# Kernel tuning notes

Measured on AMD Instinct MI355X. Metric: run time of the kernel, lower is better.

Reference implementation:

```python
import jax, jax.numpy as jnp
import numpy as np

B, D = 65536, 512
E_SPEC, E_SH = 2, 2
H1, H2, EO, TH = 64, 32, 32, 64
T1_DIM, T2_DIM = 3, 2


def _lin(key, shape, fan_in):
    bound = 1.0 / np.sqrt(fan_in)
    return jax.random.uniform(key, shape, jnp.float32, -bound, bound)


def _expert_params(key, n):
    ks = jax.random.split(key, 6)
    return (
        _lin(ks[0], (n, D, H1), D), _lin(ks[1], (n, H1), D),
        _lin(ks[2], (n, H1, H2), H1), _lin(ks[3], (n, H2), H1),
        _lin(ks[4], (n, H2, EO), H2), _lin(ks[5], (n, EO), H2),
    )


def setup_inputs() -> dict:
    key = jax.random.key(0)
    ks = jax.random.split(key, 8)
    x = jax.random.normal(ks[0], (B, D), jnp.float32)
    sh = _expert_params(ks[1], E_SH)
    t1 = _expert_params(ks[2], E_SPEC)
    t2 = _expert_params(ks[3], E_SPEC)
    EG = E_SPEC + E_SH
    g1_W, g1_b = _lin(jax.random.fold_in(ks[4], 0), (D, EG), D), _lin(jax.random.fold_in(ks[4], 1), (EG,), D)
    g2_W, g2_b = _lin(jax.random.fold_in(ks[5], 0), (D, EG), D), _lin(jax.random.fold_in(ks[5], 1), (EG,), D)
    kt = jax.random.split(ks[6], 4)
    tw1_W1, tw1_b1 = _lin(kt[0], (EO, TH), EO), _lin(kt[1], (TH,), EO)
    tw1_W2, tw1_b2 = _lin(kt[2], (TH, T1_DIM), TH), _lin(kt[3], (T1_DIM,), TH)
    kt2 = jax.random.split(ks[7], 4)
    tw2_W1, tw2_b1 = _lin(kt2[0], (EO, TH), EO), _lin(kt2[1], (TH,), EO)
    tw2_W2, tw2_b2 = _lin(kt2[2], (TH, T2_DIM), TH), _lin(kt2[3], (T2_DIM,), TH)
    return {
        "x": x,
        "sh_W1": sh[0], "sh_b1": sh[1], "sh_W2": sh[2], "sh_b2": sh[3], "sh_W3": sh[4], "sh_b3": sh[5],
        "t1_W1": t1[0], "t1_b1": t1[1], "t1_W2": t1[2], "t1_b2": t1[3], "t1_W3": t1[4], "t1_b3": t1[5],
        "t2_W1": t2[0], "t2_b1": t2[1], "t2_W2": t2[2], "t2_b2": t2[3], "t2_W3": t2[4], "t2_b3": t2[5],
        "g1_W": g1_W, "g1_b": g1_b, "g2_W": g2_W, "g2_b": g2_b,
        "tw1_W1": tw1_W1, "tw1_b1": tw1_b1, "tw1_W2": tw1_W2, "tw1_b2": tw1_b2,
        "tw2_W1": tw2_W1, "tw2_b1": tw2_b1, "tw2_W2": tw2_W2, "tw2_b2": tw2_b2,
    }


def _experts(x, W1, b1, W2, b2, W3, b3):
    # batched over expert dim e: [e, B, h] (dropout is identity in eval)
    h = jax.nn.relu(jnp.einsum('bi,eih->ebh', x, W1) + b1[:, None, :])
    h = jax.nn.relu(jnp.einsum('ebh,ehk->ebk', h, W2) + b2[:, None, :])
    return jnp.einsum('ebk,eko->ebo', h, W3) + b3[:, None, :]


def _tower(g, W1, b1, W2, b2):
    return jax.nn.relu(g @ W1 + b1) @ W2 + b2


def reference(x, sh_W1, sh_b1, sh_W2, sh_b2, sh_W3, sh_b3,
              t1_W1, t1_b1, t1_W2, t1_b2, t1_W3, t1_b3,
              t2_W1, t2_b1, t2_W2, t2_b2, t2_W3, t2_b3,
              g1_W, g1_b, g2_W, g2_b,
              tw1_W1, tw1_b1, tw1_W2, tw1_b2,
              tw2_W1, tw2_b1, tw2_W2, tw2_b2):
    shared = _experts(x, sh_W1, sh_b1, sh_W2, sh_b2, sh_W3, sh_b3)   # [E_SH, B, EO]
    task1 = _experts(x, t1_W1, t1_b1, t1_W2, t1_b2, t1_W3, t1_b3)    # [E_SPEC, B, EO]
    task2 = _experts(x, t2_W1, t2_b1, t2_W2, t2_b2, t2_W3, t2_b3)

    sel1 = jax.nn.softmax(x @ g1_W + g1_b, axis=1)                    # [B, E_SPEC+E_SH]
    g1 = jnp.einsum('ebc,be->bc', jnp.concatenate([task1, shared], 0), sel1)
    o1 = _tower(g1, tw1_W1, tw1_b1, tw1_W2, tw1_b2)
    o1 = o1.at[:, 0].set(jax.nn.sigmoid(o1[:, 0]))
    o1 = o1.at[:, 2].set(jax.nn.sigmoid(o1[:, 2]))

    sel2 = jax.nn.softmax(x @ g2_W + g2_b, axis=1)
    g2 = jnp.einsum('ebc,be->bc', jnp.concatenate([task2, shared], 0), sel2)
    o2 = _tower(g2, tw2_W1, tw2_b1, tw2_W2, tw2_b2)
    o2 = o2.at[:, 1].set(jax.nn.sigmoid(o2[:, 1]))
    return (o1, o2)
```

## Files before the change

kernel.cpp:

```cpp
#include <hip/hip_runtime.h>
#include <hip/hip_bf16.h>


#define MT 32
#define NT1 25

typedef __bf16 bf16x8 __attribute__((ext_vector_type(8)));
typedef float f32x4 __attribute__((ext_vector_type(4)));

__device__ __forceinline__ unsigned short f2bf(float f) {
    unsigned u = __builtin_bit_cast(unsigned, f);
    return (unsigned short)((u + 0x7FFFu + ((u >> 16) & 1u)) >> 16);
}
__device__ __forceinline__ unsigned pk(float a, float b) {
    return (unsigned)f2bf(a) | ((unsigned)f2bf(b) << 16);
}

__global__ void pack_all(const float* __restrict__ sh_W1, const float* __restrict__ t1_W1,
                         const float* __restrict__ t2_W1, const float* __restrict__ g1_W,
                         const float* __restrict__ g2_W,
                         const float* __restrict__ sh_W2, const float* __restrict__ t1_W2,
                         const float* __restrict__ t2_W2,
                         const float* __restrict__ sh_W3, const float* __restrict__ t1_W3,
                         const float* __restrict__ t2_W3,
                         const float* __restrict__ sh_b1, const float* __restrict__ t1_b1,
                         const float* __restrict__ t2_b1,
                         const float* __restrict__ sh_b2, const float* __restrict__ t1_b2,
                         const float* __restrict__ t2_b2,
                         const float* __restrict__ sh_b3, const float* __restrict__ t1_b3,
                         const float* __restrict__ t2_b3,
                         const float* __restrict__ g1_b, const float* __restrict__ g2_b,
                         unsigned short* __restrict__ wf1, unsigned short* __restrict__ wf2,
                         unsigned short* __restrict__ wf3,
                         float* __restrict__ b1c, float* __restrict__ b2c, float* __restrict__ b3c) {
    int p0 = blockIdx.x * blockDim.x + threadIdx.x;
    if (p0 < 204800) {
        int p = p0;
        int j = p & 7, lane = (p >> 3) & 63, ks = (p >> 9) & 15, nt = p >> 13;
        int col = nt * 16 + (lane & 15);
        int k = ks * 32 + (lane >> 4) * 8 + j;
        float v = 0.f;
        if (col < 384) {
            int e = col >> 6, ci = col & 63;
            const float* W = (e < 2) ? t1_W1 : (e < 4) ? t2_W1 : sh_W1;
            v = W[((size_t)(e & 1) * 512 + k) * 64 + ci];
        } else if (col < 388) {
            v = g1_W[k * 4 + (col - 384)];
        } else if (col < 392) {
            v = g2_W[k * 4 + (col - 388)];
        }
        wf1[p] = f2bf(v);
        return;
    }
    int p = p0 - 204800;
    if (p < 12288) {
        int j = p & 7, lane = (p >> 3) & 63, ks = (p >> 9) & 1, nt = (p >> 10) & 1, e = p >> 11;
        int col = nt * 16 + (lane & 15);
        int k = ks * 32 + (lane >> 4) * 8 + j;
        const float* W = (e < 2) ? t1_W2 : (e < 4) ? t2_W2 : sh_W2;
        wf2[p] = f2bf(W[((size_t)(e & 1) * 64 + k) * 32 + col]);
    } else if (p < 18432) {
        int q = p - 12288;
        int j = q & 7, lane = (q >> 3) & 63, nt = (q >> 9) & 1, e = q >> 10;
        int col = nt * 16 + (lane & 15);
        int k = (lane >> 4) * 8 + j;
        const float* W = (e < 2) ? t1_W3 : (e < 4) ? t2_W3 : sh_W3;
        wf3[q] = f2bf(W[((size_t)(e & 1) * 32 + k) * 32 + col]);
    } else if (p < 18432 + 392) {
        int t = p - 18432;
        float v;
        if (t < 384) {
            int e = t >> 6, ci = t & 63;
            const float* bb = (e < 2) ? t1_b1 : (e < 4) ? t2_b1 : sh_b1;
            v = bb[(e & 1) * 64 + ci];
        } else if (t < 388) v = g1_b[t - 384];
        else v = g2_b[t - 388];
        b1c[t] = v;
    } else if (p < 18824 + 192) {
        int t = p - 18824;
        int e = t >> 5, ci = t & 31;
        const float* bb = (e < 2) ? t1_b2 : (e < 4) ? t2_b2 : sh_b2;
        b2c[t] = bb[(e & 1) * 32 + ci];
    } else if (p < 19016 + 192) {
        int t = p - 19016;
        int e = t >> 5, ci = t & 31;
        const float* bb = (e < 2) ? t1_b3 : (e < 4) ? t2_b3 : sh_b3;
        b3c[t] = bb[(e & 1) * 32 + ci];
    }
}

#define LDS_BYTES 48128

__global__ __launch_bounds__(512, 6) void ple_fused(
    const float* __restrict__ x,
    const unsigned short* __restrict__ wf1, const unsigned short* __restrict__ wf2,
    const unsigned short* __restrict__ wf3,
    const float* __restrict__ b1c, const float* __restrict__ b2c, const float* __restrict__ b3c,
    const float* __restrict__ tw1_W1, const float* __restrict__ tw1_b1,
    const float* __restrict__ tw1_W2, const float* __restrict__ tw1_b2,
    const float* __restrict__ tw2_W1, const float* __restrict__ tw2_b1,
    const float* __restrict__ tw2_W2, const float* __restrict__ tw2_b2,
    float* __restrict__ out, int ntok) {
    extern __shared__ char smem[];
    unsigned short* xlds = (unsigned short*)smem;
    unsigned short* h1 = (unsigned short*)smem;
    float* eo = (float*)smem;
    float* th1 = (float*)smem;
    float* th2 = (float*)(smem + 8448);
    unsigned short* h2 = (unsigned short*)(smem + 33280);
    float* g1l = (float*)(smem + 33280);
    float* g2l = (float*)(smem + 37504);
    float* gate = (float*)(smem + 46080);
    float* sel = (float*)(smem + 47104);

    const int tid = threadIdx.x;
    const int w = tid >> 6, l = tid & 63, r = l & 15, g = l >> 4;
    const int tok0 = blockIdx.x * MT;

    const float* xb = x + (size_t)tok0 * 512;
    float4 va[8];
#pragma unroll
    for (int i = 0; i < 4; ++i) {
        va[2 * i] = *(const float4*)(xb + i * 4096 + tid * 8);
        va[2 * i + 1] = *(const float4*)(xb + i * 4096 + tid * 8 + 4);
    }
#pragma unroll
    for (int i = 0; i < 4; ++i) {
        int f = i * 4096 + tid * 8;
        int tok = f >> 9, k = f & 511;
        float4 a = va[2 * i], b = va[2 * i + 1];
        *(uint4*)(&xlds[tok * 520 + k]) =
            make_uint4(pk(a.x, a.y), pk(a.z, a.w), pk(b.x, b.y), pk(b.z, b.w));
    }
    __syncthreads();

    int ntl[4] = {w, w + 8, w + 16, 24};
    const int ntn = (w == 7) ? 4 : 3;

    f32x4 acc[4][2];
#pragma unroll
    for (int i = 0; i < 4; ++i)
#pragma unroll
        for (int m = 0; m < 2; ++m) acc[i][m] = (f32x4){0.f, 0.f, 0.f, 0.f};

    const bf16x8* wf1v = (const bf16x8*)wf1;
#pragma unroll 4
    for (int ks = 0; ks < 16; ++ks) {
        bf16x8 bfr[4];
#pragma unroll
        for (int i = 0; i < 4; ++i)
            if (i < ntn) bfr[i] = wf1v[((ntl[i] * 16 + ks) << 6) + l];
        bf16x8 afr[2];
#pragma unroll
        for (int m = 0; m < 2; ++m)
            afr[m] = *(const bf16x8*)&xlds[(m * 16 + r) * 520 + ks * 32 + g * 8];
#pragma unroll
        for (int i = 0; i < 4; ++i)
            if (i < ntn)
#pragma unroll
                for (int m = 0; m < 2; ++m)
                    acc[i][m] = __builtin_amdgcn_mfma_f32_16x16x32_bf16(afr[m], bfr[i], acc[i][m], 0, 0, 0);
    }
    __syncthreads();

#pragma unroll
    for (int i = 0; i < 4; ++i)
        if (i < ntn) {
            int nt = ntl[i];
            if (nt < 24) {
#pragma unroll
                for (int m = 0; m < 2; ++m)
#pragma unroll
                    for (int q = 0; q < 4; ++q) {
                        int tokr = m * 16 + g * 4 + q;
                        int col = nt * 16 + r;
                        float v = acc[i][m][q] + b1c[col];
                        h1[tokr * 408 + col] = f2bf(fmaxf(v, 0.f));
                    }
            } else if (r < 8) {
#pragma unroll
                for (int m = 0; m < 2; ++m)
#pragma unroll
                    for (int q = 0; q < 4; ++q) {
                        int tokr = m * 16 + g * 4 + q;
                        gate[tokr * 8 + r] = acc[i][m][q] + b1c[384 + r];
                    }
            }
        }
    __syncthreads();

    if (tid < 32) {
#pragma unroll
        for (int gi = 0; gi < 2; ++gi) {
            float l0 = gate[tid * 8 + gi * 4 + 0];
            float l1 = gate[tid * 8 + gi * 4 + 1];
            float l2 = gate[tid * 8 + gi * 4 + 2];
            float l3 = gate[tid * 8 + gi * 4 + 3];
            float mx = fmaxf(fmaxf(l0, l1), fmaxf(l2, l3));
            float e0 = __expf(l0 - mx), e1 = __expf(l1 - mx);
            float e2 = __expf(l2 - mx), e3 = __expf(l3 - mx);
            float inv = 1.f / (e0 + e1 + e2 + e3);
            sel[tid * 8 + gi * 4 + 0] = e0 * inv;
            sel[tid * 8 + gi * 4 + 1] = e1 * inv;
            sel[tid * 8 + gi * 4 + 2] = e2 * inv;
            sel[tid * 8 + gi * 4 + 3] = e3 * inv;
        }
    }

    const int nj = (w < 4) ? 2 : 1;
    const int je[2] = {w >> 1, (w + 8) >> 1};
    const int jn[2] = {w & 1, w & 1};

    f32x4 acc2[2][2];
#pragma unroll
    for (int jj = 0; jj < 2; ++jj)
#pragma unroll
        for (int m = 0; m < 2; ++m) acc2[jj][m] = (f32x4){0.f, 0.f, 0.f, 0.f};

    const bf16x8* wf2v = (const bf16x8*)wf2;
#pragma unroll
    for (int jj = 0; jj < 2; ++jj)
        if (jj < nj) {
            int e = je[jj], nt2 = jn[jj];
#pragma unroll
            for (int ks = 0; ks < 2; ++ks) {
                bf16x8 bb = wf2v[(((e * 2 + nt2) * 2 + ks) << 6) + l];
#pragma unroll
                for (int m = 0; m < 2; ++m) {
                    bf16x8 aa = *(const bf16x8*)&h1[(m * 16 + r) * 408 + e * 64 + ks * 32 + g * 8];
                    acc2[jj][m] = __builtin_amdgcn_mfma_f32_16x16x32_bf16(aa, bb, acc2[jj][m], 0, 0, 0);
                }
            }
        }
#pragma unroll
    for (int jj = 0; jj < 2; ++jj)
        if (jj < nj) {
            int e = je[jj], nt2 = jn[jj];
#pragma unroll
            for (int m = 0; m < 2; ++m)
#pragma unroll
                for (int q = 0; q < 4; ++q) {
                    int tokr = m * 16 + g * 4 + q;
                    int col = nt2 * 16 + r;
                    float v = acc2[jj][m][q] + b2c[e * 32 + col];
                    h2[tokr * 200 + e * 32 + col] = f2bf(fmaxf(v, 0.f));
                }
        }
    __syncthreads();

    f32x4 acc3[2][2];
#pragma unroll
    for (int jj = 0; jj < 2; ++jj)
#pragma unroll
        for (int m = 0; m < 2; ++m) acc3[jj][m] = (f32x4){0.f, 0.f, 0.f, 0.f};

    const bf16x8* wf3v = (const bf16x8*)wf3;
#pragma unroll
    for (int jj = 0; jj < 2; ++jj)
        if (jj < nj) {
            int e = je[jj], nt2 = jn[jj];
            bf16x8 bb = wf3v[((e * 2 + nt2) << 6) + l];
#pragma unroll
            for (int m = 0; m < 2; ++m) {
                bf16x8 aa = *(const bf16x8*)&h2[(m * 16 + r) * 200 + e * 32 + g * 8];
                acc3[jj][m] = __builtin_amdgcn_mfma_f32_16x16x32_bf16(aa, bb, acc3[jj][m], 0, 0, 0);
            }
        }
#pragma unroll
    for (int jj = 0; jj < 2; ++jj)
        if (jj < nj) {
            int e = je[jj], nt2 = jn[jj];
#pragma unroll
            for (int m = 0; m < 2; ++m)
#pragma unroll
                for (int q = 0; q < 4; ++q) {
                    int tokr = m * 16 + g * 4 + q;
                    eo[(e * 32 + tokr) * 33 + nt2 * 16 + r] =
                        acc3[jj][m][q] + b3c[e * 32 + nt2 * 16 + r];
                }
        }
    __syncthreads();

    {
        int tok = tid >> 4, c0 = (tid & 15) * 2;
        float s[8];
#pragma unroll
        for (int i = 0; i < 8; ++i) s[i] = sel[tok * 8 + i];
#pragma unroll
        for (int c = 0; c < 2; ++c) {
            int cc = c0 + c;
            float e0 = eo[(0 * 32 + tok) * 33 + cc];
            float e1 = eo[(1 * 32 + tok) * 33 + cc];
            float e2 = eo[(2 * 32 + tok) * 33 + cc];
            float e3 = eo[(3 * 32 + tok) * 33 + cc];
            float e4 = eo[(4 * 32 + tok) * 33 + cc];
            float e5 = eo[(5 * 32 + tok) * 33 + cc];
            g1l[tok * 33 + cc] = s[0] * e0 + s[1] * e1 + s[2] * e4 + s[3] * e5;
            g2l[tok * 33 + cc] = s[4] * e2 + s[5] * e3 + s[6] * e4 + s[7] * e5;
        }
    }
    __syncthreads();

    {
        int tt = tid & 255, tower = tid >> 8;
        int tok = tt >> 3, h0 = (tt & 7) * 8;
        const float* W1 = tower ? tw2_W1 : tw1_W1;
        const float* B1 = tower ? tw2_b1 : tw1_b1;
        const float* gl = tower ? g2l : g1l;
        float* th = tower ? th2 : th1;
        float a[8];
#pragma unroll
        for (int hh = 0; hh < 8; ++hh) a[hh] = B1[h0 + hh];
        for (int c = 0; c < 32; ++c) {
            float gv = gl[tok * 33 + c];
#pragma unroll
            for (int hh = 0; hh < 8; ++hh)
                a[hh] += gv * W1[c * 64 + h0 + hh];
        }
#pragma unroll
        for (int hh = 0; hh < 8; ++hh)
            th[tok * 66 + h0 + hh] = fmaxf(a[hh], 0.f);
    }
    __syncthreads();

    if (tid < 128) {
        int tok = tid >> 2, jx = tid & 3;
        if (jx < 3) {
            float s = tw1_b2[jx];
            for (int hh = 0; hh < 64; ++hh) s += th1[tok * 66 + hh] * tw1_W2[hh * 3 + jx];
            if (jx != 1) s = 1.f / (1.f + __expf(-s));
            out[(size_t)(tok0 + tok) * 3 + jx] = s;
        }
    } else if (tid >= 256 && tid < 384) {
        int t2 = tid - 256, tok = t2 >> 2, jx = t2 & 3;
        if (jx < 2) {
            float s = tw2_b2[jx];
            for (int hh = 0; hh < 64; ++hh) s += th2[tok * 66 + hh] * tw2_W2[hh * 2 + jx];
            if (jx == 1) s = 1.f / (1.f + __expf(-s));
            out[(size_t)ntok * 3 + (size_t)(tok0 + tok) * 2 + jx] = s;
        }
    }
}

extern "C" void kernel_launch(void* const* d_in, const int* in_sizes, int n_in,
                              void* d_out, int out_size, void* d_ws, size_t ws_size,
                              hipStream_t stream) {
    const float* x = (const float*)d_in[0];
    const float* sh_W1 = (const float*)d_in[1];
    const float* sh_b1 = (const float*)d_in[2];
    const float* sh_W2 = (const float*)d_in[3];
    const float* sh_b2 = (const float*)d_in[4];
    const float* sh_W3 = (const float*)d_in[5];
    const float* sh_b3 = (const float*)d_in[6];
    const float* t1_W1 = (const float*)d_in[7];
    const float* t1_b1 = (const float*)d_in[8];
    const float* t1_W2 = (const float*)d_in[9];
    const float* t1_b2 = (const float*)d_in[10];
    const float* t1_W3 = (const float*)d_in[11];
    const float* t1_b3 = (const float*)d_in[12];
    const float* t2_W1 = (const float*)d_in[13];
    const float* t2_b1 = (const float*)d_in[14];
    const float* t2_W2 = (const float*)d_in[15];
    const float* t2_b2 = (const float*)d_in[16];
    const float* t2_W3 = (const float*)d_in[17];
    const float* t2_b3 = (const float*)d_in[18];
    const float* g1_W = (const float*)d_in[19];
    const float* g1_b = (const float*)d_in[20];
    const float* g2_W = (const float*)d_in[21];
    const float* g2_b = (const float*)d_in[22];
    const float* tw1_W1 = (const float*)d_in[23];
    const float* tw1_b1 = (const float*)d_in[24];
    const float* tw1_W2 = (const float*)d_in[25];
    const float* tw1_b2 = (const float*)d_in[26];
    const float* tw2_W1 = (const float*)d_in[27];
    const float* tw2_b1 = (const float*)d_in[28];
    const float* tw2_W2 = (const float*)d_in[29];
    const float* tw2_b2 = (const float*)d_in[30];

    unsigned short* wf1 = (unsigned short*)d_ws;
    unsigned short* wf2 = (unsigned short*)((char*)d_ws + 409600);
    unsigned short* wf3 = (unsigned short*)((char*)d_ws + 434176);
    float* b1c = (float*)((char*)d_ws + 446464);
    float* b2c = (float*)((char*)d_ws + 448032);
    float* b3c = (float*)((char*)d_ws + 448800);

    pack_all<<<438, 512, 0, stream>>>(sh_W1, t1_W1, t2_W1, g1_W, g2_W,
                                      sh_W2, t1_W2, t2_W2, sh_W3, t1_W3, t2_W3,
                                      sh_b1, t1_b1, t2_b1, sh_b2, t1_b2, t2_b2,
                                      sh_b3, t1_b3, t2_b3, g1_b, g2_b,
                                      wf1, wf2, wf3, b1c, b2c, b3c);

    (void)hipFuncSetAttribute((const void*)ple_fused,
                              hipFuncAttributeMaxDynamicSharedMemorySize, LDS_BYTES);

    int ntok = in_sizes[0] / 512;
    int nblk = ntok / MT;
    ple_fused<<<nblk, 512, LDS_BYTES, stream>>>(
        x, wf1, wf2, wf3, b1c, b2c, b3c,
        tw1_W1, tw1_b1, tw1_W2, tw1_b2, tw2_W1, tw2_b1, tw2_W2, tw2_b2,
        (float*)d_out, ntok);
}
```

Before: 310.4 us.

## Give each wave one expert's full MLP chain in private LDS slabs

Work is reassigned so each of six waves computes a whole expert (layer1→layer2→layer3) in its own LDS slab, and the two remaining waves compute the gate logits. This removes several block-wide barriers between the expert layers. The softmax is now computed redundantly per thread inside the mixing step instead of in a separate 32-thread phase. In exchange, LDS use grows enough that launch bounds drop from 6 to 4 blocks, and the waves carry uneven load: the gate waves do far less work than the expert waves.

```diff
diff --git a/kernel.cpp b/kernel.cpp
--- a/kernel.cpp
+++ b/kernel.cpp
@@ -89,9 +89,11 @@
     }
 }
 
-#define LDS_BYTES 48128
-
-__global__ __launch_bounds__(512, 6) void ple_fused(
+#define SLAB_OFF 33280
+#define SLAB_SZ  7168
+#define LDS_BYTES 77312
+
+__global__ __launch_bounds__(512, 4) void ple_fused(
     const float* __restrict__ x,
     const unsigned short* __restrict__ wf1, const unsigned short* __restrict__ wf2,
     const unsigned short* __restrict__ wf3,
@@ -103,200 +105,179 @@
     float* __restrict__ out, int ntok) {
     extern __shared__ char smem[];
     unsigned short* xlds = (unsigned short*)smem;
-    unsigned short* h1 = (unsigned short*)smem;
-    float* eo = (float*)smem;
-    float* th1 = (float*)smem;
-    float* th2 = (float*)(smem + 8448);
-    unsigned short* h2 = (unsigned short*)(smem + 33280);
-    float* g1l = (float*)(smem + 33280);
-    float* g2l = (float*)(smem + 37504);
-    float* gate = (float*)(smem + 46080);
-    float* sel = (float*)(smem + 47104);
+    float* gate = (float*)(smem + 76288);
+    float* g1l = (float*)smem;
+    float* g2l = (float*)(smem + 4224);
+    float* th1 = (float*)(smem + 8448);
+    float* th2 = (float*)(smem + 16896);
 
     const int tid = threadIdx.x;
     const int w = tid >> 6, l = tid & 63, r = l & 15, g = l >> 4;
     const int tok0 = blockIdx.x * MT;
 
-    const float* xb = x + (size_t)tok0 * 512;
-    float4 va[8];
-#pragma unroll
-    for (int i = 0; i < 4; ++i) {
-        va[2 * i] = *(const float4*)(xb + i * 4096 + tid * 8);
-        va[2 * i + 1] = *(const float4*)(xb + i * 4096 + tid * 8 + 4);
-    }
-#pragma unroll
-    for (int i = 0; i < 4; ++i) {
-        int f = i * 4096 + tid * 8;
-        int tok = f >> 9, k = f & 511;
-        float4 a = va[2 * i], b = va[2 * i + 1];
-        *(uint4*)(&xlds[tok * 520 + k]) =
-            make_uint4(pk(a.x, a.y), pk(a.z, a.w), pk(b.x, b.y), pk(b.z, b.w));
+    {
+        const float* xb = x + (size_t)tok0 * 512;
+        float4 va[8];
+#pragma unroll
+        for (int i = 0; i < 4; ++i) {
+            va[2 * i] = *(const float4*)(xb + i * 4096 + tid * 8);
+            va[2 * i + 1] = *(const float4*)(xb + i * 4096 + tid * 8 + 4);
+        }
+#pragma unroll
+        for (int i = 0; i < 4; ++i) {
+            int f = i * 4096 + tid * 8;
+            int tok = f >> 9, k = f & 511;
+            float4 a = va[2 * i], b = va[2 * i + 1];
+            *(uint4*)(&xlds[tok * 520 + k]) =
+                make_uint4(pk(a.x, a.y), pk(a.z, a.w), pk(b.x, b.y), pk(b.z, b.w));
+        }
     }
     __syncthreads();
 
-    int ntl[4] = {w, w + 8, w + 16, 24};
-    const int ntn = (w == 7) ? 4 : 3;
-
-    f32x4 acc[4][2];
-#pragma unroll
-    for (int i = 0; i < 4; ++i)
-#pragma unroll
-        for (int m = 0; m < 2; ++m) acc[i][m] = (f32x4){0.f, 0.f, 0.f, 0.f};
-
     const bf16x8* wf1v = (const bf16x8*)wf1;
+    if (w < 6) {
+        const int e = w;
+        unsigned short* h1w = (unsigned short*)(smem + SLAB_OFF + w * SLAB_SZ);
+        unsigned short* h2w = (unsigned short*)(smem + SLAB_OFF + w * SLAB_SZ + 4608);
+        float* eow = (float*)(smem + SLAB_OFF + w * SLAB_SZ);
+
+        f32x4 acc[4][2];
+#pragma unroll
+        for (int i = 0; i < 4; ++i)
+#pragma unroll
+            for (int m = 0; m < 2; ++m) acc[i][m] = (f32x4){0.f, 0.f, 0.f, 0.f};
+
 #pragma unroll 4
-    for (int ks = 0; ks < 16; ++ks) {
-        bf16x8 bfr[4];
-#pragma unroll
-        for (int i = 0; i < 4; ++i)
-            if (i < ntn) bfr[i] = wf1v[((ntl[i] * 16 + ks) << 6) + l];
-        bf16x8 afr[2];
-#pragma unroll
-        for (int m = 0; m < 2; ++m)
-            afr[m] = *(const bf16x8*)&xlds[(m * 16 + r) * 520 + ks * 32 + g * 8];
-#pragma unroll
-        for (int i = 0; i < 4; ++i)
-            if (i < ntn)
+        for (int ks = 0; ks < 16; ++ks) {
+            bf16x8 bfr[4];
+#pragma unroll
+            for (int i = 0; i < 4; ++i)
+                bfr[i] = wf1v[(((e * 4 + i) * 16 + ks) << 6) + l];
+            bf16x8 afr[2];
+#pragma unroll
+            for (int m = 0; m < 2; ++m)
+                afr[m] = *(const bf16x8*)&xlds[(m * 16 + r) * 520 + ks * 32 + g * 8];
+#pragma unroll
+            for (int i = 0; i < 4; ++i)
 #pragma unroll
                 for (int m = 0; m < 2; ++m)
                     acc[i][m] = __builtin_amdgcn_mfma_f32_16x16x32_bf16(afr[m], bfr[i], acc[i][m], 0, 0, 0);
-    }
-    __syncthreads();
-
-#pragma unroll
-    for (int i = 0; i < 4; ++i)
-        if (i < ntn) {
-            int nt = ntl[i];
-            if (nt < 24) {
+        }
+#pragma unroll
+        for (int i = 0; i < 4; ++i)
+#pragma unroll
+            for (int m = 0; m < 2; ++m)
+#pragma unroll
+                for (int q = 0; q < 4; ++q) {
+                    float v = acc[i][m][q] + b1c[e * 64 + i * 16 + r];
+                    h1w[(m * 16 + g * 4 + q) * 72 + i * 16 + r] = f2bf(fmaxf(v, 0.f));
+                }
+
+        const bf16x8* wf2v = (const bf16x8*)wf2;
+        f32x4 acc2[2][2];
+#pragma unroll
+        for (int i = 0; i < 2; ++i)
+#pragma unroll
+            for (int m = 0; m < 2; ++m) acc2[i][m] = (f32x4){0.f, 0.f, 0.f, 0.f};
+#pragma unroll
+        for (int ks = 0; ks < 2; ++ks) {
+            bf16x8 aa[2];
+#pragma unroll
+            for (int m = 0; m < 2; ++m)
+                aa[m] = *(const bf16x8*)&h1w[(m * 16 + r) * 72 + ks * 32 + g * 8];
+#pragma unroll
+            for (int i = 0; i < 2; ++i) {
+                bf16x8 bb = wf2v[(((e * 2 + i) * 2 + ks) << 6) + l];
 #pragma unroll
                 for (int m = 0; m < 2; ++m)
-#pragma unroll
-                    for (int q = 0; q < 4; ++q) {
-                        int tokr = m * 16 + g * 4 + q;
-                        int col = nt * 16 + r;
-                        float v = acc[i][m][q] + b1c[col];
-                        h1[tokr * 408 + col] = f2bf(fmaxf(v, 0.f));
-                    }
-            } else if (r < 8) {
+                    acc2[i][m] = __builtin_amdgcn_mfma_f32_16x16x32_bf16(aa[m], bb, acc2[i][m], 0, 0, 0);
+            }
+        }
+#pragma unroll
+        for (int i = 0; i < 2; ++i)
+#pragma unroll
+            for (int m = 0; m < 2; ++m)
+#pragma unroll
+                for (int q = 0; q < 4; ++q) {
+                    float v = acc2[i][m][q] + b2c[e * 32 + i * 16 + r];
+                    h2w[(m * 16 + g * 4 + q) * 40 + i * 16 + r] = f2bf(fmaxf(v, 0.f));
+                }
+
+        const bf16x8* wf3v = (const bf16x8*)wf3;
+        f32x4 acc3[2][2];
+#pragma unroll
+        for (int i = 0; i < 2; ++i)
+#pragma unroll
+            for (int m = 0; m < 2; ++m) acc3[i][m] = (f32x4){0.f, 0.f, 0.f, 0.f};
+        {
+            bf16x8 aa[2];
+#pragma unroll
+            for (int m = 0; m < 2; ++m)
+                aa[m] = *(const bf16x8*)&h2w[(m * 16 + r) * 40 + g * 8];
+#pragma unroll
+            for (int i = 0; i < 2; ++i) {
+                bf16x8 bb = wf3v[((e * 2 + i) << 6) + l];
 #pragma unroll
                 for (int m = 0; m < 2; ++m)
-#pragma unroll
-                    for (int q = 0; q < 4; ++q) {
-                        int tokr = m * 16 + g * 4 + q;
-                        gate[tokr * 8 + r] = acc[i][m][q] + b1c[384 + r];
-                    }
+                    acc3[i][m] = __builtin_amdgcn_mfma_f32_16x16x32_bf16(aa[m], bb, acc3[i][m], 0, 0, 0);
             }
         }
-    __syncthreads();
-
-    if (tid < 32) {
-#pragma unroll
-        for (int gi = 0; gi < 2; ++gi) {
-            float l0 = gate[tid * 8 + gi * 4 + 0];
-            float l1 = gate[tid * 8 + gi * 4 + 1];
-            float l2 = gate[tid * 8 + gi * 4 + 2];
-            float l3 = gate[tid * 8 + gi * 4 + 3];
-            float mx = fmaxf(fmaxf(l0, l1), fmaxf(l2, l3));
-            float e0 = __expf(l0 - mx), e1 = __expf(l1 - mx);
-            float e2 = __expf(l2 - mx), e3 = __expf(l3 - mx);
-            float inv = 1.f / (e0 + e1 + e2 + e3);
-            sel[tid * 8 + gi * 4 + 0] = e0 * inv;
-            sel[tid * 8 + gi * 4 + 1] = e1 * inv;
-            sel[tid * 8 + gi * 4 + 2] = e2 * inv;
-            sel[tid * 8 + gi * 4 + 3] = e3 * inv;
-        }
-    }
-
-    const int nj = (w < 4) ? 2 : 1;
-    const int je[2] = {w >> 1, (w + 8) >> 1};
-    const int jn[2] = {w & 1, w & 1};
-
-    f32x4 acc2[2][2];
-#pragma unroll
-    for (int jj = 0; jj < 2; ++jj)
-#pragma unroll
-        for (int m = 0; m < 2; ++m) acc2[jj][m] = (f32x4){0.f, 0.f, 0.f, 0.f};
-
-    const bf16x8* wf2v = (const bf16x8*)wf2;
-#pragma unroll
-    for (int jj = 0; jj < 2; ++jj)
-        if (jj < nj) {
-            int e = je[jj], nt2 = jn[jj];
-#pragma unroll
-            for (int ks = 0; ks < 2; ++ks) {
-                bf16x8 bb = wf2v[(((e * 2 + nt2) * 2 + ks) << 6) + l];
-#pragma unroll
-                for (int m = 0; m < 2; ++m) {
-                    bf16x8 aa = *(const bf16x8*)&h1[(m * 16 + r) * 408 + e * 64 + ks * 32 + g * 8];
-                    acc2[jj][m] = __builtin_amdgcn_mfma_f32_16x16x32_bf16(aa, bb, acc2[jj][m], 0, 0, 0);
-                }
-            }
-        }
-#pragma unroll
-    for (int jj = 0; jj < 2; ++jj)
-        if (jj < nj) {
-            int e = je[jj], nt2 = jn[jj];
-#pragma unroll
-            for (int m = 0; m < 2; ++m)
-#pragma unroll
-                for (int q = 0; q < 4; ++q) {
-                    int tokr = m * 16 + g * 4 + q;
-                    int col = nt2 * 16 + r;
-                    float v = acc2[jj][m][q] + b2c[e * 32 + col];
-                    h2[tokr * 200 + e * 32 + col] = f2bf(fmaxf(v, 0.f));
-                }
-        }
-    __syncthreads();
-
-    f32x4 acc3[2][2];
-#pragma unroll
-    for (int jj = 0; jj < 2; ++jj)
-#pragma unroll
-        for (int m = 0; m < 2; ++m) acc3[jj][m] = (f32x4){0.f, 0.f, 0.f, 0.f};
-
-    const bf16x8* wf3v = (const bf16x8*)wf3;
-#pragma unroll
-    for (int jj = 0; jj < 2; ++jj)
-        if (jj < nj) {
-            int e = je[jj], nt2 = jn[jj];
-            bf16x8 bb = wf3v[((e * 2 + nt2) << 6) + l];
-#pragma unroll
-            for (int m = 0; m < 2; ++m) {
-                bf16x8 aa = *(const bf16x8*)&h2[(m * 16 + r) * 200 + e * 32 + g * 8];
-                acc3[jj][m] = __builtin_amdgcn_mfma_f32_16x16x32_bf16(aa, bb, acc3[jj][m], 0, 0, 0);
-            }
-        }
-#pragma unroll
-    for (int jj = 0; jj < 2; ++jj)
-        if (jj < nj) {
-            int e = je[jj], nt2 = jn[jj];
-#pragma unroll
-            for (int m = 0; m < 2; ++m)
-#pragma unroll
-                for (int q = 0; q < 4; ++q) {
-                    int tokr = m * 16 + g * 4 + q;
-                    eo[(e * 32 + tokr) * 33 + nt2 * 16 + r] =
-                        acc3[jj][m][q] + b3c[e * 32 + nt2 * 16 + r];
-                }
-        }
+#pragma unroll
+        for (int i = 0; i < 2; ++i)
+#pragma unroll
+            for (int m = 0; m < 2; ++m)
+#pragma unroll
+                for (int q = 0; q < 4; ++q)
+                    eow[(m * 16 + g * 4 + q) * 33 + i * 16 + r] =
+                        acc3[i][m][q] + b3c[e * 32 + i * 16 + r];
+    } else {
+        const int m = w - 6;
+        f32x4 accg = (f32x4){0.f, 0.f, 0.f, 0.f};
+#pragma unroll 4
+        for (int ks = 0; ks < 16; ++ks) {
+            bf16x8 bfr = wf1v[((24 * 16 + ks) << 6) + l];
+            bf16x8 afr = *(const bf16x8*)&xlds[(m * 16 + r) * 520 + ks * 32 + g * 8];
+            accg = __builtin_amdgcn_mfma_f32_16x16x32_bf16(afr, bfr, accg, 0, 0, 0);
+        }
+        if (r < 8) {
+#pragma unroll
+            for (int q = 0; q < 4; ++q)
+                gate[(m * 16 + g * 4 + q) * 8 + r] = accg[q] + b1c[384 + r];
+        }
+    }
     __syncthreads();
 
     {
         int tok = tid >> 4, c0 = (tid & 15) * 2;
-        float s[8];
-#pragma unroll
-        for (int i = 0; i < 8; ++i) s[i] = sel[tok * 8 + i];
+        float lg[8];
+#pragma unroll
+        for (int i = 0; i < 8; ++i) lg[i] = gate[tok * 8 + i];
+        float mx1 = fmaxf(fmaxf(lg[0], lg[1]), fmaxf(lg[2], lg[3]));
+        float mx2 = fmaxf(fmaxf(lg[4], lg[5]), fmaxf(lg[6], lg[7]));
+        float s1[4], s2[4];
+        float d1 = 0.f, d2 = 0.f;
+#pragma unroll
+        for (int i = 0; i < 4; ++i) { s1[i] = __expf(lg[i] - mx1); d1 += s1[i]; }
+#pragma unroll
+        for (int i = 0; i < 4; ++i) { s2[i] = __expf(lg[4 + i] - mx2); d2 += s2[i]; }
+        float inv1 = 1.f / d1, inv2 = 1.f / d2;
+#pragma unroll
+        for (int i = 0; i < 4; ++i) { s1[i] *= inv1; s2[i] *= inv2; }
+
 #pragma unroll
         for (int c = 0; c < 2; ++c) {
             int cc = c0 + c;
-            float e0 = eo[(0 * 32 + tok) * 33 + cc];
-            float e1 = eo[(1 * 32 + tok) * 33 + cc];
-            float e2 = eo[(2 * 32 + tok) * 33 + cc];
-            float e3 = eo[(3 * 32 + tok) * 33 + cc];
-            float e4 = eo[(4 * 32 + tok) * 33 + cc];
-            float e5 = eo[(5 * 32 + tok) * 33 + cc];
-            g1l[tok * 33 + cc] = s[0] * e0 + s[1] * e1 + s[2] * e4 + s[3] * e5;
-            g2l[tok * 33 + cc] = s[4] * e2 + s[5] * e3 + s[6] * e4 + s[7] * e5;
+            const float* eo0 = (const float*)(smem + SLAB_OFF + 0 * SLAB_SZ);
+            const float* eo1 = (const float*)(smem + SLAB_OFF + 1 * SLAB_SZ);
+            const float* eo2 = (const float*)(smem + SLAB_OFF + 2 * SLAB_SZ);
+            const float* eo3 = (const float*)(smem + SLAB_OFF + 3 * SLAB_SZ);
+            const float* eo4 = (const float*)(smem + SLAB_OFF + 4 * SLAB_SZ);
+            const float* eo5 = (const float*)(smem + SLAB_OFF + 5 * SLAB_SZ);
+            float v0 = eo0[tok * 33 + cc], v1 = eo1[tok * 33 + cc];
+            float v2 = eo2[tok * 33 + cc], v3 = eo3[tok * 33 + cc];
+            float v4 = eo4[tok * 33 + cc], v5 = eo5[tok * 33 + cc];
+            g1l[tok * 33 + cc] = s1[0] * v0 + s1[1] * v1 + s1[2] * v4 + s1[3] * v5;
+            g2l[tok * 33 + cc] = s2[0] * v2 + s2[1] * v3 + s2[2] * v4 + s2[3] * v5;
         }
     }
     __syncthreads();
```

Measured after the change: 311.3 us. No clear change (+0.3%).
